# Kernel tuning notes

Measured on AMD Instinct MI355X. Metric: run time of the kernel, lower is better.

Reference implementation:

```python
import jax, jax.numpy as jnp
import numpy as np

B, N, K, T, H = 4, 1024, 100, 2, 64
NFEAT = 96  # ntypes * m1 * m2 = 2 * 12 * 4


def setup_inputs() -> dict:
    key = jax.random.key(0)
    ks = jax.random.split(key, 8)
    feat = jax.random.normal(ks[0], (B, N, NFEAT), jnp.float32)
    dfeat = jax.random.normal(ks[1], (B, N, K, NFEAT, 3), jnp.float32) * 0.1
    ImageDR = jax.random.uniform(ks[2], (B, N, K, 4), jnp.float32)
    # 1-based neighbor indices; 0 marks an empty (padded) neighbor slot
    list_neigh_alltype = jax.random.randint(ks[3], (B, N, K), 0, N + 1).astype(jnp.int32)
    Imagetype_map = jnp.sort(jax.random.randint(ks[4], (N,), 0, T)).astype(jnp.int32)
    # per-type FittingNet params: 96 -> 64 -> 64 (resnet w/ resnet_dt) -> 1
    W1 = jax.random.normal(ks[5], (T, NFEAT, H), jnp.float32) * (1.0 / np.sqrt(NFEAT))
    b1 = jnp.zeros((T, H), jnp.float32)
    W2 = jax.random.normal(ks[6], (T, H, H), jnp.float32) * (1.0 / np.sqrt(H))
    b2 = jnp.zeros((T, H), jnp.float32)
    rdt = jnp.full((T, H), 0.1, jnp.float32)  # resnet_dt timestep params
    Wout = jax.random.normal(ks[7], (T, H), jnp.float32) * (1.0 / np.sqrt(H))
    bout = jnp.array([-3.2, -5.1], jnp.float32)  # per-type energy shift
    return dict(feat=feat, dfeat=dfeat, ImageDR=ImageDR,
                list_neigh_alltype=list_neigh_alltype, Imagetype_map=Imagetype_map,
                W1=W1, b1=b1, W2=W2, b2=b2, rdt=rdt, Wout=Wout, bout=bout, nghost=0)


def _fitting_Ei(feat, Imagetype_map, W1, b1, W2, b2, rdt, Wout, bout):
    # Evaluate every per-type fitting net on all atoms, then select by atom type.
    h1 = jnp.tanh(jnp.einsum('bnf,tfh->tbnh', feat, W1) + b1[:, None, None, :])
    h2 = h1 + rdt[:, None, None, :] * jnp.tanh(
        jnp.einsum('tbnh,thg->tbng', h1, W2) + b2[:, None, None, :])
    e = jnp.einsum('tbnh,th->tbn', h2, Wout) + bout[:, None, None]  # (T,B,N)
    sel = Imagetype_map.astype(jnp.int32)[None, :, None]            # (1,N,1)
    Ei = jnp.take_along_axis(e.transpose(1, 2, 0), sel, axis=2)[..., 0]  # (B,N)
    return Ei


def reference(feat, dfeat, ImageDR, list_neigh_alltype, Imagetype_map,
              W1, b1, W2, b2, rdt, Wout, bout, nghost):
    # Ei and dE/dfeat (the torch code uses autograd.grad on Ei wrt feat)
    Ei, vjp_fn = jax.vjp(
        lambda f: _fitting_Ei(f, Imagetype_map, W1, b1, W2, b2, rdt, Wout, bout), feat)
    Etot = Ei.sum(axis=1)                                    # (B,)
    dE = vjp_fn(jnp.ones_like(Ei))[0]                        # (B,N,NFEAT)
    # dE_dfeat[b,i,k,:] = sum_f dE[b,i,f] * dfeat[b,i,k,f,:]
    dE_dfeat = jnp.einsum('bnf,bnkfx->bnkx', dE, dfeat)      # (B,N,K,3)
    valid = (list_neigh_alltype > 0).astype(dE_dfeat.dtype)[..., None]
    pair_f = dE_dfeat * valid
    # force buffer sized natoms + nghost + 1; slot 0 absorbs padded neighbors
    Fbuf = jnp.zeros((B, N + 1 + nghost, 3), dE_dfeat.dtype)
    bidx = jnp.arange(B)[:, None, None]
    Fbuf = Fbuf.at[bidx, list_neigh_alltype].add(pair_f)     # scatter to neighbors
    Fbuf = Fbuf.at[:, 1:N + 1, :].add(-pair_f.sum(axis=2))   # center-atom reaction
    Force = Fbuf[:, 1:N + 1, :]                              # (B,N,3)
    rij = ImageDR[..., 1:4]                                  # (B,N,K,3)
    Virial = -jnp.einsum('bnkx,bnky->bxy', rij, pair_f).reshape(B, 9)
    return Etot, Ei, Force, Virial
```

## Files before the change

kernel.cpp:

```cpp
#include <hip/hip_runtime.h>

#define BB 4
#define NN 1024
#define KK 100
#define HH 64
#define FF 96

#define OFF_EI   4
#define OFF_F    (4 + BB*NN)
#define OFF_VIR  (OFF_F + BB*NN*3)
#define OUT_TOT  (OFF_VIR + BB*9)

__device__ __forceinline__ float wave_sum(float v) {
    #pragma unroll
    for (int off = 32; off > 0; off >>= 1)
        v += __shfl_xor(v, off, 64);
    return v;
}

__global__ __launch_bounds__(256) void zero_kernel(float* __restrict__ out) {
    int i = blockIdx.x * 256 + threadIdx.x;
    if (i < OUT_TOT) out[i] = 0.f;
}

__global__ __launch_bounds__(256) void fused_kernel(
    const float* __restrict__ feat, const int* __restrict__ tmap,
    const float* __restrict__ W1, const float* __restrict__ b1,
    const float* __restrict__ W2, const float* __restrict__ b2,
    const float* __restrict__ rdt, const float* __restrict__ Wout,
    const float* __restrict__ bout,
    const float* __restrict__ dfeat, const float* __restrict__ ImageDR,
    const int* __restrict__ neigh, float* __restrict__ out)
{
    const int row  = blockIdx.x;
    const int b    = row / NN;
    const int n    = row - b * NN;
    const int tid  = threadIdx.x;
    const int wave = tid >> 6;
    const int lane = tid & 63;

    __shared__ float sdE[FF];
    __shared__ float sdr[KK * 4];
    __shared__ int   snb[KK];
    __shared__ float swf[4][3];
    __shared__ float svir[4][9];

    const float* drbase = ImageDR + (size_t)row * (KK * 4);
    for (int i = tid; i < KK * 4; i += 256) sdr[i] = drbase[i];
    if (tid < KK) snb[tid] = neigh[(size_t)row * KK + tid];

    if (wave == 0) {
        const int t = tmap[n];
        const float* frow = feat + (size_t)row * FF;
        const float* W1t  = W1 + (size_t)t * FF * HH;
        const float* W2t  = W2 + (size_t)t * HH * HH;

        float f0 = frow[lane];
        float f1 = (lane < 32) ? frow[HH + lane] : 0.f;

        float z1 = b1[t * HH + lane];
        #pragma unroll 8
        for (int f = 0; f < HH; ++f)
            z1 = fmaf(__shfl(f0, f, 64), W1t[f * HH + lane], z1);
        #pragma unroll 8
        for (int f = 0; f < FF - HH; ++f)
            z1 = fmaf(__shfl(f1, f, 64), W1t[(HH + f) * HH + lane], z1);
        float h1 = tanhf(z1);

        float z2 = b2[t * HH + lane];
        #pragma unroll 8
        for (int h = 0; h < HH; ++h)
            z2 = fmaf(__shfl(h1, h, 64), W2t[h * HH + lane], z2);
        float u  = tanhf(z2);
        float r  = rdt[t * HH + lane];
        float wo = Wout[t * HH + lane];

        float e = wave_sum((h1 + r * u) * wo);

        float dz2 = r * wo * (1.f - u * u);
        float dh1 = wo;
        #pragma unroll 8
        for (int g = 0; g < HH; ++g)
            dh1 = fmaf(__shfl(dz2, g, 64), W2t[lane * HH + g], dh1);
        float dz1 = dh1 * (1.f - h1 * h1);

        float acc0 = 0.f, acc1 = 0.f;
        #pragma unroll 8
        for (int h = 0; h < HH; ++h) {
            const float d = __shfl(dz1, h, 64);
            acc0 = fmaf(d, W1t[lane * HH + h], acc0);
            if (lane < 32) acc1 = fmaf(d, W1t[(HH + lane) * HH + h], acc1);
        }
        sdE[lane] = acc0;
        if (lane < 32) sdE[HH + lane] = acc1;

        if (lane == 0) {
            const float Ei = e + bout[t];
            out[OFF_EI + row] = Ei;
            atomicAdd(&out[b], Ei);
        }
    }
    __syncthreads();

    const float w0 = sdE[lane];
    const float w1 = (lane < 32) ? sdE[HH + lane] : 0.f;

    float sacc0 = 0.f, sacc1 = 0.f, sacc2 = 0.f;
    float vacc  = 0.f;
    const int vx = lane / 3, vy = lane - 3 * vx;

    const size_t pbase = (size_t)row * KK;

    #pragma unroll 2
    for (int k = wave; k < KK; k += 4) {
        const float* dfp = dfeat + (pbase + k) * (FF * 3);
        float a0 = dfp[lane * 3 + 0] * w0;
        float a1 = dfp[lane * 3 + 1] * w0;
        float a2 = dfp[lane * 3 + 2] * w0;
        if (lane < 32) {
            const int m = (HH + lane) * 3;
            a0 = fmaf(dfp[m + 0], w1, a0);
            a1 = fmaf(dfp[m + 1], w1, a1);
            a2 = fmaf(dfp[m + 2], w1, a2);
        }
        float pf0 = wave_sum(a0);
        float pf1 = wave_sum(a1);
        float pf2 = wave_sum(a2);

        const int j = snb[k];
        if (j <= 0) { pf0 = 0.f; pf1 = 0.f; pf2 = 0.f; }
        else if (lane < 3) {
            const float v = (lane == 0) ? pf0 : ((lane == 1) ? pf1 : pf2);
            atomicAdd(&out[OFF_F + ((size_t)b * NN + (j - 1)) * 3 + lane], v);
        }

        sacc0 -= pf0; sacc1 -= pf1; sacc2 -= pf2;

        if (lane < 9) {
            const float rx  = sdr[k * 4 + 1 + vx];
            const float pfy = (vy == 0) ? pf0 : ((vy == 1) ? pf1 : pf2);
            vacc = fmaf(-rx, pfy, vacc);
        }
    }

    if (lane < 3) swf[wave][lane]  = (lane == 0) ? sacc0 : ((lane == 1) ? sacc1 : sacc2);
    if (lane < 9) svir[wave][lane] = vacc;
    __syncthreads();

    if (tid < 3) atomicAdd(&out[OFF_F + (size_t)row * 3 + tid],
                           swf[0][tid] + swf[1][tid] + swf[2][tid] + swf[3][tid]);
    if (tid < 9) atomicAdd(&out[OFF_VIR + b * 9 + tid],
                           svir[0][tid] + svir[1][tid] + svir[2][tid] + svir[3][tid]);
}

extern "C" void kernel_launch(void* const* d_in, const int* in_sizes, int n_in,
                              void* d_out, int out_size, void* d_ws, size_t ws_size,
                              hipStream_t stream) {
    const float* feat    = (const float*)d_in[0];
    const float* dfeat   = (const float*)d_in[1];
    const float* ImageDR = (const float*)d_in[2];
    const int*   neigh   = (const int*)  d_in[3];
    const int*   tmap    = (const int*)  d_in[4];
    const float* W1      = (const float*)d_in[5];
    const float* b1      = (const float*)d_in[6];
    const float* W2      = (const float*)d_in[7];
    const float* b2      = (const float*)d_in[8];
    const float* rdt     = (const float*)d_in[9];
    const float* Wout    = (const float*)d_in[10];
    const float* bout    = (const float*)d_in[11];

    float* out = (float*)d_out;

    zero_kernel<<<(OUT_TOT + 255) / 256, 256, 0, stream>>>(out);
    fused_kernel<<<BB * NN, 256, 0, stream>>>(feat, tmap, W1, b1, W2, b2, rdt,
                                              Wout, bout, dfeat, ImageDR, neigh, out);
}
```

Baseline: 741.6 us.

## Replicate fitting-net per wave, pre-transpose weights, and split neighbors into contiguous chunks

A prep kernel now also writes transposed copies of W1 and W2 into the workspace. This makes the backward-pass weight reads coalesced across lanes instead of strided by HH. Every wave now computes the fitting net and dE/dfeat redundantly, which removes the block barriers, the shared-memory hand-off and the idle waves during the MLP phase. Each wave handles a contiguous 25-neighbor chunk and issues its own force and virial atomics. The cost is four times the MLP arithmetic per block and four times as many per-row atomics.

```diff
diff --git a/kernel.cpp b/kernel.cpp
--- a/kernel.cpp
+++ b/kernel.cpp
@@ -3,13 +3,19 @@
 #define BB 4
 #define NN 1024
 #define KK 100
+#define TT 2
 #define HH 64
 #define FF 96
+#define KPW 25
 
 #define OFF_EI   4
 #define OFF_F    (4 + BB*NN)
 #define OFF_VIR  (OFF_F + BB*NN*3)
 #define OUT_TOT  (OFF_VIR + BB*9)
+
+#define WS_W1T   0
+#define WS_W2T   (TT*HH*FF)
+#define PREP_MAX ((OUT_TOT > TT*FF*HH) ? OUT_TOT : TT*FF*HH)
 
 __device__ __forceinline__ float wave_sum(float v) {
     #pragma unroll
@@ -18,9 +24,24 @@
     return v;
 }
 
-__global__ __launch_bounds__(256) void zero_kernel(float* __restrict__ out) {
+__global__ __launch_bounds__(256) void prep_kernel(
+    const float* __restrict__ W1, const float* __restrict__ W2,
+    float* __restrict__ ws, float* __restrict__ out)
+{
     int i = blockIdx.x * 256 + threadIdx.x;
     if (i < OUT_TOT) out[i] = 0.f;
+    float* W1T = ws + WS_W1T;
+    float* W2T = ws + WS_W2T;
+    if (i < TT * FF * HH) {
+        int t = i / (FF * HH), r = i % (FF * HH);
+        int f = r / HH, h = r % HH;
+        W1T[(t * HH + h) * FF + f] = W1[i];
+    }
+    if (i < TT * HH * HH) {
+        int t = i / (HH * HH), r = i % (HH * HH);
+        int h = r / HH, g = r % HH;
+        W2T[(t * HH + g) * HH + h] = W2[i];
+    }
 }
 
 __global__ __launch_bounds__(256) void fused_kernel(
@@ -28,7 +49,7 @@
     const float* __restrict__ W1, const float* __restrict__ b1,
     const float* __restrict__ W2, const float* __restrict__ b2,
     const float* __restrict__ rdt, const float* __restrict__ Wout,
-    const float* __restrict__ bout,
+    const float* __restrict__ bout, const float* __restrict__ ws,
     const float* __restrict__ dfeat, const float* __restrict__ ImageDR,
     const int* __restrict__ neigh, float* __restrict__ out)
 {
@@ -38,72 +59,68 @@
     const int tid  = threadIdx.x;
     const int wave = tid >> 6;
     const int lane = tid & 63;
+    const int k0   = wave * KPW;
 
-    __shared__ float sdE[FF];
     __shared__ float sdr[KK * 4];
     __shared__ int   snb[KK];
-    __shared__ float swf[4][3];
-    __shared__ float svir[4][9];
 
-    const float* drbase = ImageDR + (size_t)row * (KK * 4);
-    for (int i = tid; i < KK * 4; i += 256) sdr[i] = drbase[i];
-    if (tid < KK) snb[tid] = neigh[(size_t)row * KK + tid];
+    {
+        const float* drbase = ImageDR + (size_t)row * (KK * 4);
+        for (int i = lane; i < KPW * 4; i += 64)
+            sdr[k0 * 4 + i] = drbase[k0 * 4 + i];
+        if (lane < KPW)
+            snb[k0 + lane] = neigh[(size_t)row * KK + k0 + lane];
+    }
 
-    if (wave == 0) {
-        const int t = tmap[n];
-        const float* frow = feat + (size_t)row * FF;
-        const float* W1t  = W1 + (size_t)t * FF * HH;
-        const float* W2t  = W2 + (size_t)t * HH * HH;
+    const int t = tmap[n];
+    const float* frow = feat + (size_t)row * FF;
+    const float* W1t  = W1 + (size_t)t * FF * HH;
+    const float* W2t  = W2 + (size_t)t * HH * HH;
+    const float* W1Tt = ws + WS_W1T + (size_t)t * HH * FF;
+    const float* W2Tt = ws + WS_W2T + (size_t)t * HH * HH;
 
-        float f0 = frow[lane];
-        float f1 = (lane < 32) ? frow[HH + lane] : 0.f;
+    float f0 = frow[lane];
+    float f1 = (lane < 32) ? frow[HH + lane] : 0.f;
 
-        float z1 = b1[t * HH + lane];
-        #pragma unroll 8
-        for (int f = 0; f < HH; ++f)
-            z1 = fmaf(__shfl(f0, f, 64), W1t[f * HH + lane], z1);
-        #pragma unroll 8
-        for (int f = 0; f < FF - HH; ++f)
-            z1 = fmaf(__shfl(f1, f, 64), W1t[(HH + f) * HH + lane], z1);
-        float h1 = tanhf(z1);
+    float z1 = b1[t * HH + lane];
+    #pragma unroll 8
+    for (int f = 0; f < HH; ++f)
+        z1 = fmaf(__shfl(f0, f, 64), W1t[f * HH + lane], z1);
+    #pragma unroll 8
+    for (int f = 0; f < FF - HH; ++f)
+        z1 = fmaf(__shfl(f1, f, 64), W1t[(HH + f) * HH + lane], z1);
+    float h1 = tanhf(z1);
 
-        float z2 = b2[t * HH + lane];
-        #pragma unroll 8
-        for (int h = 0; h < HH; ++h)
-            z2 = fmaf(__shfl(h1, h, 64), W2t[h * HH + lane], z2);
-        float u  = tanhf(z2);
-        float r  = rdt[t * HH + lane];
-        float wo = Wout[t * HH + lane];
+    float z2 = b2[t * HH + lane];
+    #pragma unroll 8
+    for (int h = 0; h < HH; ++h)
+        z2 = fmaf(__shfl(h1, h, 64), W2t[h * HH + lane], z2);
+    float u  = tanhf(z2);
+    float r  = rdt[t * HH + lane];
+    float wo = Wout[t * HH + lane];
 
-        float e = wave_sum((h1 + r * u) * wo);
+    float e = wave_sum((h1 + r * u) * wo);
 
-        float dz2 = r * wo * (1.f - u * u);
-        float dh1 = wo;
-        #pragma unroll 8
-        for (int g = 0; g < HH; ++g)
-            dh1 = fmaf(__shfl(dz2, g, 64), W2t[lane * HH + g], dh1);
-        float dz1 = dh1 * (1.f - h1 * h1);
+    float dz2 = r * wo * (1.f - u * u);
+    float dh1 = wo;
+    #pragma unroll 8
+    for (int g = 0; g < HH; ++g)
+        dh1 = fmaf(__shfl(dz2, g, 64), W2Tt[g * HH + lane], dh1);
+    float dz1 = dh1 * (1.f - h1 * h1);
 
-        float acc0 = 0.f, acc1 = 0.f;
-        #pragma unroll 8
-        for (int h = 0; h < HH; ++h) {
-            const float d = __shfl(dz1, h, 64);
-            acc0 = fmaf(d, W1t[lane * HH + h], acc0);
-            if (lane < 32) acc1 = fmaf(d, W1t[(HH + lane) * HH + h], acc1);
-        }
-        sdE[lane] = acc0;
-        if (lane < 32) sdE[HH + lane] = acc1;
+    float w0 = 0.f, w1 = 0.f;
+    #pragma unroll 8
+    for (int h = 0; h < HH; ++h) {
+        const float d = __shfl(dz1, h, 64);
+        w0 = fmaf(d, W1Tt[h * FF + lane], w0);
+        if (lane < 32) w1 = fmaf(d, W1Tt[h * FF + HH + lane], w1);
+    }
 
-        if (lane == 0) {
-            const float Ei = e + bout[t];
-            out[OFF_EI + row] = Ei;
-            atomicAdd(&out[b], Ei);
-        }
+    if (wave == 0 && lane == 0) {
+        const float Ei = e + bout[t];
+        out[OFF_EI + row] = Ei;
+        atomicAdd(&out[b], Ei);
     }
-    __syncthreads();
-
-    const float w0 = sdE[lane];
-    const float w1 = (lane < 32) ? sdE[HH + lane] : 0.f;
 
     float sacc0 = 0.f, sacc1 = 0.f, sacc2 = 0.f;
     float vacc  = 0.f;
@@ -112,7 +129,7 @@
     const size_t pbase = (size_t)row * KK;
 
     #pragma unroll 2
-    for (int k = wave; k < KK; k += 4) {
+    for (int k = k0; k < k0 + KPW; ++k) {
         const float* dfp = dfeat + (pbase + k) * (FF * 3);
         float a0 = dfp[lane * 3 + 0] * w0;
         float a1 = dfp[lane * 3 + 1] * w0;
@@ -143,14 +160,11 @@
         }
     }
 
-    if (lane < 3) swf[wave][lane]  = (lane == 0) ? sacc0 : ((lane == 1) ? sacc1 : sacc2);
-    if (lane < 9) svir[wave][lane] = vacc;
-    __syncthreads();
-
-    if (tid < 3) atomicAdd(&out[OFF_F + (size_t)row * 3 + tid],
-                           swf[0][tid] + swf[1][tid] + swf[2][tid] + swf[3][tid]);
-    if (tid < 9) atomicAdd(&out[OFF_VIR + b * 9 + tid],
-                           svir[0][tid] + svir[1][tid] + svir[2][tid] + svir[3][tid]);
+    if (lane < 3) {
+        const float s = (lane == 0) ? sacc0 : ((lane == 1) ? sacc1 : sacc2);
+        atomicAdd(&out[OFF_F + (size_t)row * 3 + lane], s);
+    }
+    if (lane < 9) atomicAdd(&out[OFF_VIR + b * 9 + lane], vacc);
 }
 
 extern "C" void kernel_launch(void* const* d_in, const int* in_sizes, int n_in,
@@ -170,8 +184,10 @@
     const float* bout    = (const float*)d_in[11];
 
     float* out = (float*)d_out;
+    float* ws  = (float*)d_ws;
 
-    zero_kernel<<<(OUT_TOT + 255) / 256, 256, 0, stream>>>(out);
+    prep_kernel<<<(PREP_MAX + 255) / 256, 256, 0, stream>>>(W1, W2, ws, out);
     fused_kernel<<<BB * NN, 256, 0, stream>>>(feat, tmap, W1, b1, W2, b2, rdt,
-                                              Wout, bout, dfeat, ImageDR, neigh, out);
+                                              Wout, bout, ws, dfeat, ImageDR,
+                                              neigh, out);
 }
```

After: 879.1 us. 18.5% more time.
